# Kernel tuning notes

Hardware: AMD Instinct MI355X
Metric: run time of the kernel (lower is better)

Reference implementation:

```python
import jax, jax.numpy as jnp
import numpy as np

N_NODES = 100000
N_EDGES = 1600000
IN_C = 128
HID = 128
OUT_C = 10
N_GRAPHS = 512


def setup_inputs() -> dict:
    key = jax.random.key(0)
    ks = jax.random.split(key, 12)
    x = jax.random.normal(ks[0], (N_NODES, IN_C), dtype=jnp.float32)
    edge_index = jax.random.randint(ks[1], (2, N_EDGES), 0, N_NODES, dtype=jnp.int64)
    batch = jnp.sort(jax.random.randint(ks[2], (N_NODES,), 0, N_GRAPHS, dtype=jnp.int64))

    def lin(k, fan_in, fan_out):
        bound = 1.0 / np.sqrt(fan_in)
        return jax.random.uniform(k, (fan_in, fan_out), jnp.float32, -bound, bound)

    params = {
        # GraphConv layer i: W_rel (neighbor aggregate transform, with bias),
        # W_root (self transform, no bias) -- matches PyG GraphConv.
        "W1_rel": lin(ks[3], IN_C, HID), "b1": jnp.zeros((HID,), jnp.float32), "W1_root": lin(ks[4], IN_C, HID),
        "W2_rel": lin(ks[5], HID, HID), "b2": jnp.zeros((HID,), jnp.float32), "W2_root": lin(ks[6], HID, HID),
        "W3_rel": lin(ks[7], HID, HID), "b3": jnp.zeros((HID,), jnp.float32), "W3_root": lin(ks[8], HID, HID),
        "W_lin": lin(ks[9], HID, OUT_C), "b_lin": jnp.zeros((OUT_C,), jnp.float32),
    }
    return {"x": x, "edge_index": edge_index, "batch": batch, **params}


def _graph_conv(x, src, dst, W_rel, b, W_root):
    # PyG GraphConv with aggr='add': out_i = W_rel @ sum_{j->i} x_j + b + W_root @ x_i
    agg = jax.ops.segment_sum(x[src], dst, num_segments=x.shape[0])  # [N, d]
    return agg @ W_rel + b + x @ W_root


def reference(x, edge_index, batch,
              W1_rel, b1, W1_root,
              W2_rel, b2, W2_root,
              W3_rel, b3, W3_root,
              W_lin, b_lin):
    src, dst = edge_index[0], edge_index[1]
    h = jax.nn.relu(_graph_conv(x, src, dst, W1_rel, b1, W1_root))
    h = jax.nn.relu(_graph_conv(h, src, dst, W2_rel, b2, W2_root))
    h = _graph_conv(h, src, dst, W3_rel, b3, W3_root)
    # global mean pool over graphs
    sums = jax.ops.segment_sum(h, batch, num_segments=N_GRAPHS)             # [G, d]
    counts = jax.ops.segment_sum(jnp.ones((h.shape[0],), h.dtype), batch, num_segments=N_GRAPHS)
    pooled = sums / jnp.maximum(counts, 1.0)[:, None]
    return pooled @ W_lin + b_lin  # [G, OUT_C]
```

## Files before the change

### kernel.cpp

```cpp
#include <hip/hip_runtime.h>

static constexpr int NN = 100000;
static constexpr int NE = 1600000;
static constexpr int C  = 128;
static constexpr int OC = 10;
static constexpr int NG = 512;

static constexpr int BSH  = 9;
static constexpr int BNW  = 1 << BSH;
static constexpr int BK   = (NN + BNW - 1) / BNW;
static constexpr int BCAP = 12288;
static constexpr int EPB  = 8192;
static constexpr int ABLK = (NE + EPB - 1) / EPB;

static constexpr int TSTRIDE = 132;

typedef unsigned short u16;
typedef __attribute__((ext_vector_type(8))) short short8;
typedef __attribute__((ext_vector_type(8))) short bf16x8;
typedef __attribute__((ext_vector_type(4))) float f32x4;

__device__ __forceinline__ float bf2f(u16 u) {
    union { float f; unsigned int u32; } v; v.u32 = ((unsigned int)u) << 16; return v.f;
}
__device__ __forceinline__ u16 f2bf(float f) {
    union { float f; unsigned int u; } v; v.f = f;
    unsigned int u = v.u;
    unsigned int r = u + 0x7FFF + ((u >> 16) & 1);
    return (u16)(r >> 16);
}

__global__ __launch_bounds__(256) void k_binA(const int* __restrict__ src,
                                              const int* __restrict__ dst,
                                              int* __restrict__ gcnt,
                                              int* __restrict__ buck) {
    __shared__ int cnt[BK];
    __shared__ int curs[BK];
    int tid = threadIdx.x;
    for (int i = tid; i < BK; i += 256) cnt[i] = 0;
    __syncthreads();
    int e0 = blockIdx.x * EPB;
    for (int i = tid; i < EPB; i += 256) {
        int e = e0 + i;
        if (e < NE) atomicAdd(&cnt[dst[e] >> BSH], 1);
    }
    __syncthreads();
    for (int i = tid; i < BK; i += 256) {
        int c = cnt[i];
        int gb = (c > 0) ? atomicAdd(&gcnt[i], c) : 0;
        curs[i] = i * BCAP + gb;
    }
    __syncthreads();
    for (int i = tid; i < EPB; i += 256) {
        int e = e0 + i;
        if (e < NE) {
            int d = dst[e];
            int b = d >> BSH;
            int p = atomicAdd(&curs[b], 1);
            if (p < (b + 1) * BCAP)
                buck[p] = (src[e] << BSH) | (d & (BNW - 1));
        }
    }
}

__global__ void k_binscan(const int* __restrict__ gcnt, int* __restrict__ csrbase,
                          int* __restrict__ rp) {
    __shared__ int buf[256];
    int tid = threadIdx.x;
    int v = (tid < BK) ? gcnt[tid] : 0;
    buf[tid] = v;
    __syncthreads();
    for (int off = 1; off < 256; off <<= 1) {
        int t = (tid >= off) ? buf[tid - off] : 0;
        __syncthreads();
        buf[tid] += t;
        __syncthreads();
    }
    if (tid < BK) csrbase[tid] = buf[tid] - v;
    if (tid == 0) rp[NN] = NE;
}

__global__ __launch_bounds__(BNW) void k_binB(const int* __restrict__ gcnt,
                                              const int* __restrict__ csrbase,
                                              const int* __restrict__ buck,
                                              int* __restrict__ rp,
                                              int* __restrict__ csr) {
    int b = blockIdx.x;
    int tid = threadIdx.x;
    __shared__ int hist[BNW];
    __shared__ int scanbuf[BNW];
    int n = gcnt[b];
    if (n > BCAP) n = BCAP;
    int base = csrbase[b];
    const int* bb = buck + (size_t)b * BCAP;

    hist[tid] = 0;
    __syncthreads();
    for (int i = tid; i < n; i += BNW) atomicAdd(&hist[bb[i] & (BNW - 1)], 1);
    __syncthreads();

    int v = hist[tid];
    scanbuf[tid] = v;
    __syncthreads();
    for (int off = 1; off < BNW; off <<= 1) {
        int t = (tid >= off) ? scanbuf[tid - off] : 0;
        __syncthreads();
        scanbuf[tid] += t;
        __syncthreads();
    }
    int excl = scanbuf[tid] - v;
    int node = (b << BSH) + tid;
    if (node < NN) rp[node] = base + excl;
    __syncthreads();
    hist[tid] = base + excl;
    __syncthreads();
    for (int i = tid; i < n; i += BNW) {
        int en = bb[i];
        int p = atomicAdd(&hist[en & (BNW - 1)], 1);
        csr[p] = en >> BSH;
    }
}

__global__ void k_cvt_bf16(const float* __restrict__ in, u16* __restrict__ out) {
    int i = blockIdx.x * blockDim.x + threadIdx.x;
    size_t base = (size_t)i * 8;
    if (base >= (size_t)NN * C) return;
    float4 a = *reinterpret_cast<const float4*>(in + base);
    float4 b = *reinterpret_cast<const float4*>(in + base + 4);
    u16 o[8] = { f2bf(a.x), f2bf(a.y), f2bf(a.z), f2bf(a.w),
                 f2bf(b.x), f2bf(b.y), f2bf(b.z), f2bf(b.w) };
    *reinterpret_cast<short8*>(out + base) = *reinterpret_cast<const short8*>(o);
}

__global__ void k_pack_w(const float* __restrict__ W_rel,
                         const float* __restrict__ W_root,
                         u16* __restrict__ Bp) {
    int t = blockIdx.x * blockDim.x + threadIdx.x;
    if (t >= 4096) return;
    int lane = t & 63;
    int nfrag = (t >> 6) & 7;
    int kk = t >> 9;
    int col = nfrag * 16 + (lane & 15);
    int k0 = kk * 32 + (lane >> 4) * 8;
    u16 vals[8];
#pragma unroll
    for (int j = 0; j < 8; ++j) {
        int k = k0 + j;
        float w = (k < C) ? W_rel[k * C + col] : W_root[(k - C) * C + col];
        vals[j] = f2bf(w);
    }
    *reinterpret_cast<short8*>(Bp + (size_t)t * 8) = *reinterpret_cast<const short8*>(vals);
}

__global__ void k_gather(const u16* __restrict__ h, const int* __restrict__ rp,
                         const int* __restrict__ csr, u16* __restrict__ agg) {
    int t = blockIdx.x * blockDim.x + threadIdx.x;
    int node = t >> 4;
    if (node >= NN) return;
    int seg = (t & 15) * 8;
    int beg = rp[node], end = rp[node + 1];
    float acc[8] = {};
    int j = beg;
    for (; j + 4 <= end; j += 4) {
        int s0 = csr[j];
        int s1 = csr[j + 1];
        int s2 = csr[j + 2];
        int s3 = csr[j + 3];
        short8 v0 = *reinterpret_cast<const short8*>(h + (size_t)s0 * C + seg);
        short8 v1 = *reinterpret_cast<const short8*>(h + (size_t)s1 * C + seg);
        short8 v2 = *reinterpret_cast<const short8*>(h + (size_t)s2 * C + seg);
        short8 v3 = *reinterpret_cast<const short8*>(h + (size_t)s3 * C + seg);
#pragma unroll
        for (int q = 0; q < 8; ++q) {
            acc[q] += bf2f((u16)v0[q]);
            acc[q] += bf2f((u16)v1[q]);
            acc[q] += bf2f((u16)v2[q]);
            acc[q] += bf2f((u16)v3[q]);
        }
    }
    for (; j < end; ++j) {
        int s = csr[j];
        short8 v = *reinterpret_cast<const short8*>(h + (size_t)s * C + seg);
#pragma unroll
        for (int q = 0; q < 8; ++q) acc[q] += bf2f((u16)v[q]);
    }
    u16 o[8];
#pragma unroll
    for (int q = 0; q < 8; ++q) o[q] = f2bf(acc[q]);
    *reinterpret_cast<short8*>(agg + (size_t)node * C + seg) = *reinterpret_cast<const short8*>(o);
}

template <bool RELU>
__global__ __launch_bounds__(256) void k_transform_mfma(
    const u16* __restrict__ agg, const u16* __restrict__ h,
    const u16* __restrict__ Bp, const float* __restrict__ bias,
    u16* __restrict__ out) {
    __shared__ u16 tile[4][16 * TSTRIDE];
    int wave = threadIdx.x >> 6;
    int lane = threadIdx.x & 63;
    int row0 = blockIdx.x * 64 + wave * 16;
    int arow = row0 + (lane & 15);
    int rclamp = arow < NN ? arow : NN - 1;
    int koff = (lane >> 4) * 8;

    f32x4 acc[8] = {};
#pragma unroll
    for (int kk = 0; kk < 8; ++kk) {
        bf16x8 a;
        if (kk < 4) {
            a = *reinterpret_cast<const bf16x8*>(agg + (size_t)rclamp * C + kk * 32 + koff);
        } else {
            a = *reinterpret_cast<const bf16x8*>(h + (size_t)rclamp * C + (kk - 4) * 32 + koff);
        }
        const u16* bp = Bp + ((size_t)kk * 8 * 64 + lane) * 8;
#pragma unroll
        for (int n = 0; n < 8; ++n) {
            bf16x8 b = *reinterpret_cast<const bf16x8*>(bp + (size_t)n * 64 * 8);
            acc[n] = __builtin_amdgcn_mfma_f32_16x16x32_bf16(a, b, acc[n], 0, 0, 0);
        }
    }

    u16* T = tile[wave];
    int colbase = lane & 15;
    int rloc = (lane >> 4) * 4;
#pragma unroll
    for (int n = 0; n < 8; ++n) {
        int col = n * 16 + colbase;
        float bb = bias[col];
#pragma unroll
        for (int r = 0; r < 4; ++r) {
            float v = acc[n][r] + bb;
            if (RELU) v = fmaxf(v, 0.0f);
            T[(rloc + r) * TSTRIDE + col] = f2bf(v);
        }
    }
    __syncthreads();

#pragma unroll
    for (int k = 0; k < 4; ++k) {
        int idx = k * 64 + lane;
        int lr = idx >> 4;
        int off = (idx & 15) * 8;
        int ro = row0 + lr;
        if (ro < NN) {
            short8 v = *reinterpret_cast<const short8*>(&T[lr * TSTRIDE + off]);
            *reinterpret_cast<short8*>(out + (size_t)ro * C + off) = v;
        }
    }
}

__global__ void k_gbounds(const int* __restrict__ batch, int* __restrict__ gstart) {
    int g = blockIdx.x * blockDim.x + threadIdx.x;
    if (g > NG) return;
    int lo = 0, hi = NN;
    while (lo < hi) { int mid = (lo + hi) >> 1; if (batch[mid] < g) lo = mid + 1; else hi = mid; }
    gstart[g] = lo;
}

__global__ __launch_bounds__(256) void k_pool_final(
    const u16* __restrict__ h, const int* __restrict__ gstart,
    const float* __restrict__ W_lin, const float* __restrict__ b_lin,
    float* __restrict__ out) {
    int g = blockIdx.x;
    int rowslot = threadIdx.x >> 4;
    int seg = threadIdx.x & 15;
    int s = gstart[g], e = gstart[g + 1];

    float acc[8] = {};
    for (int i = s + rowslot; i < e; i += 16) {
        short8 v = *reinterpret_cast<const short8*>(h + (size_t)i * C + seg * 8);
#pragma unroll
        for (int q = 0; q < 8; ++q) acc[q] += bf2f((u16)v[q]);
    }

    __shared__ float red[16][C];
#pragma unroll
    for (int q = 0; q < 8; ++q) red[rowslot][seg * 8 + q] = acc[q];
    __syncthreads();

    __shared__ float sp[C];
    if (threadIdx.x < C) {
        float sum = 0.0f;
#pragma unroll
        for (int r = 0; r < 16; ++r) sum += red[r][threadIdx.x];
        float cnt = (float)max(e - s, 1);
        sp[threadIdx.x] = sum / cnt;
    }
    __syncthreads();
    if (threadIdx.x < OC) {
        float o = b_lin[threadIdx.x];
#pragma unroll 8
        for (int k = 0; k < C; ++k) o += sp[k] * W_lin[k * OC + threadIdx.x];
        out[g * OC + threadIdx.x] = o;
    }
}

extern "C" void kernel_launch(void* const* d_in, const int* in_sizes, int n_in,
                              void* d_out, int out_size, void* d_ws, size_t ws_size,
                              hipStream_t stream) {
    const float* x       = (const float*)d_in[0];
    const int*   eidx    = (const int*)d_in[1];
    const int*   batch   = (const int*)d_in[2];
    const float* W1_rel  = (const float*)d_in[3];
    const float* b1      = (const float*)d_in[4];
    const float* W1_root = (const float*)d_in[5];
    const float* W2_rel  = (const float*)d_in[6];
    const float* b2      = (const float*)d_in[7];
    const float* W2_root = (const float*)d_in[8];
    const float* W3_rel  = (const float*)d_in[9];
    const float* b3      = (const float*)d_in[10];
    const float* W3_root = (const float*)d_in[11];
    const float* W_lin   = (const float*)d_in[12];
    const float* b_lin   = (const float*)d_in[13];
    float* out = (float*)d_out;

    const int* src = eidx;
    const int* dst = eidx + NE;

    u16* xb   = (u16*)d_ws;
    u16* hb   = xb + (size_t)NN * C;
    u16* aggb = hb + (size_t)NN * C;
    u16* Bp   = aggb + (size_t)NN * C;
    int* rp      = (int*)(Bp + 3 * 32768);
    int* csr     = rp + NN + 1;
    int* buck    = csr + NE;
    int* gcnt    = buck + (size_t)BK * BCAP;
    int* csrbase = gcnt + BK;
    int* gstart  = csrbase + BK;

    const int gb = (NN * 16 + 255) / 256;
    const int tb = (NN + 63) / 64;
    const int cvtb = ((NN * C / 8) + 255) / 256;

    hipMemsetAsync(gcnt, 0, BK * sizeof(int), stream);
    k_binA<<<ABLK, 256, 0, stream>>>(src, dst, gcnt, buck);
    k_binscan<<<1, 256, 0, stream>>>(gcnt, csrbase, rp);
    k_binB<<<BK, BNW, 0, stream>>>(gcnt, csrbase, buck, rp, csr);

    k_cvt_bf16<<<cvtb, 256, 0, stream>>>(x, xb);
    k_pack_w<<<16, 256, 0, stream>>>(W1_rel, W1_root, Bp);
    k_pack_w<<<16, 256, 0, stream>>>(W2_rel, W2_root, Bp + 32768);
    k_pack_w<<<16, 256, 0, stream>>>(W3_rel, W3_root, Bp + 2 * 32768);
    k_gbounds<<<3, 256, 0, stream>>>(batch, gstart);

    k_gather<<<gb, 256, 0, stream>>>(xb, rp, csr, aggb);
    k_transform_mfma<true><<<tb, 256, 0, stream>>>(aggb, xb, Bp, b1, hb);

    k_gather<<<gb, 256, 0, stream>>>(hb, rp, csr, aggb);
    k_transform_mfma<true><<<tb, 256, 0, stream>>>(aggb, hb, Bp + 32768, b2, hb);

    k_gather<<<gb, 256, 0, stream>>>(hb, rp, csr, aggb);
    k_transform_mfma<false><<<tb, 256, 0, stream>>>(aggb, hb, Bp + 2 * 32768, b3, hb);

    k_pool_final<<<NG, 256, 0, stream>>>(hb, gstart, W_lin, b_lin, out);
}
```

Baseline: 343.2 us.

## Use a full wavefront per node in gather and merge small setup kernels

The gather kernel now assigns 64 lanes per node instead of 16. Four edge groups load neighbor rows in parallel, and the partial sums are combined with cross-lane shuffles before one quarter of the wave writes the result. This exposes more memory-level parallelism on the irregular neighbor gathers, in exchange for shuffle overhead and idle lanes on low-degree nodes. Separately, the bin scan is merged with the graph-bounds search, and the weight packing is merged with the bf16 conversion, which cuts the number of kernel launches.

```diff
diff --git a/kernel.cpp b/kernel.cpp
--- a/kernel.cpp
+++ b/kernel.cpp
@@ -63,21 +63,32 @@
     }
 }
 
-__global__ void k_binscan(const int* __restrict__ gcnt, int* __restrict__ csrbase,
-                          int* __restrict__ rp) {
-    __shared__ int buf[256];
+__global__ __launch_bounds__(256) void k_meta(const int* __restrict__ gcnt,
+                                              int* __restrict__ csrbase,
+                                              int* __restrict__ rp,
+                                              const int* __restrict__ batch,
+                                              int* __restrict__ gstart) {
     int tid = threadIdx.x;
-    int v = (tid < BK) ? gcnt[tid] : 0;
-    buf[tid] = v;
-    __syncthreads();
-    for (int off = 1; off < 256; off <<= 1) {
-        int t = (tid >= off) ? buf[tid - off] : 0;
+    if (blockIdx.x == 0) {
+        __shared__ int buf[256];
+        int v = (tid < BK) ? gcnt[tid] : 0;
+        buf[tid] = v;
         __syncthreads();
-        buf[tid] += t;
-        __syncthreads();
-    }
-    if (tid < BK) csrbase[tid] = buf[tid] - v;
-    if (tid == 0) rp[NN] = NE;
+        for (int off = 1; off < 256; off <<= 1) {
+            int t = (tid >= off) ? buf[tid - off] : 0;
+            __syncthreads();
+            buf[tid] += t;
+            __syncthreads();
+        }
+        if (tid < BK) csrbase[tid] = buf[tid] - v;
+        if (tid == 0) rp[NN] = NE;
+    } else {
+        int g = (blockIdx.x - 1) * 256 + tid;
+        if (g > NG) return;
+        int lo = 0, hi = NN;
+        while (lo < hi) { int mid = (lo + hi) >> 1; if (batch[mid] < g) lo = mid + 1; else hi = mid; }
+        gstart[g] = lo;
+    }
 }
 
 __global__ __launch_bounds__(BNW) void k_binB(const int* __restrict__ gcnt,
@@ -121,73 +132,98 @@
     }
 }
 
-__global__ void k_cvt_bf16(const float* __restrict__ in, u16* __restrict__ out) {
-    int i = blockIdx.x * blockDim.x + threadIdx.x;
-    size_t base = (size_t)i * 8;
-    if (base >= (size_t)NN * C) return;
-    float4 a = *reinterpret_cast<const float4*>(in + base);
-    float4 b = *reinterpret_cast<const float4*>(in + base + 4);
-    u16 o[8] = { f2bf(a.x), f2bf(a.y), f2bf(a.z), f2bf(a.w),
-                 f2bf(b.x), f2bf(b.y), f2bf(b.z), f2bf(b.w) };
-    *reinterpret_cast<short8*>(out + base) = *reinterpret_cast<const short8*>(o);
-}
-
-__global__ void k_pack_w(const float* __restrict__ W_rel,
-                         const float* __restrict__ W_root,
-                         u16* __restrict__ Bp) {
+__global__ __launch_bounds__(256) void k_prep(
+    const float* __restrict__ x, u16* __restrict__ xb,
+    const float* __restrict__ W1r, const float* __restrict__ W1o,
+    const float* __restrict__ W2r, const float* __restrict__ W2o,
+    const float* __restrict__ W3r, const float* __restrict__ W3o,
+    u16* __restrict__ Bp) {
+    int bid = blockIdx.x;
+    if (bid < 48) {
+        int layer = bid >> 4;
+        const float* Wr = (layer == 0) ? W1r : (layer == 1) ? W2r : W3r;
+        const float* Wo = (layer == 0) ? W1o : (layer == 1) ? W2o : W3o;
+        u16* out = Bp + layer * 32768;
+        int t = (bid & 15) * 256 + threadIdx.x;
+        int lane = t & 63;
+        int nfrag = (t >> 6) & 7;
+        int kk = t >> 9;
+        int col = nfrag * 16 + (lane & 15);
+        int k0 = kk * 32 + (lane >> 4) * 8;
+        u16 vals[8];
+#pragma unroll
+        for (int j = 0; j < 8; ++j) {
+            int k = k0 + j;
+            float w = (k < C) ? Wr[k * C + col] : Wo[(k - C) * C + col];
+            vals[j] = f2bf(w);
+        }
+        *reinterpret_cast<short8*>(out + (size_t)t * 8) = *reinterpret_cast<const short8*>(vals);
+    } else {
+        int i = (bid - 48) * 256 + threadIdx.x;
+        size_t base = (size_t)i * 8;
+        if (base >= (size_t)NN * C) return;
+        float4 a = *reinterpret_cast<const float4*>(x + base);
+        float4 b = *reinterpret_cast<const float4*>(x + base + 4);
+        u16 o[8] = { f2bf(a.x), f2bf(a.y), f2bf(a.z), f2bf(a.w),
+                     f2bf(b.x), f2bf(b.y), f2bf(b.z), f2bf(b.w) };
+        *reinterpret_cast<short8*>(xb + base) = *reinterpret_cast<const short8*>(o);
+    }
+}
+
+__global__ __launch_bounds__(256) void k_gather(const u16* __restrict__ h,
+                                                const int* __restrict__ rp,
+                                                const int* __restrict__ csr,
+                                                u16* __restrict__ agg) {
     int t = blockIdx.x * blockDim.x + threadIdx.x;
-    if (t >= 4096) return;
+    int node = t >> 6;
+    if (node >= NN) return;
     int lane = t & 63;
-    int nfrag = (t >> 6) & 7;
-    int kk = t >> 9;
-    int col = nfrag * 16 + (lane & 15);
-    int k0 = kk * 32 + (lane >> 4) * 8;
-    u16 vals[8];
-#pragma unroll
-    for (int j = 0; j < 8; ++j) {
-        int k = k0 + j;
-        float w = (k < C) ? W_rel[k * C + col] : W_root[(k - C) * C + col];
-        vals[j] = f2bf(w);
-    }
-    *reinterpret_cast<short8*>(Bp + (size_t)t * 8) = *reinterpret_cast<const short8*>(vals);
-}
-
-__global__ void k_gather(const u16* __restrict__ h, const int* __restrict__ rp,
-                         const int* __restrict__ csr, u16* __restrict__ agg) {
-    int t = blockIdx.x * blockDim.x + threadIdx.x;
-    int node = t >> 4;
-    if (node >= NN) return;
-    int seg = (t & 15) * 8;
+    int jj = lane >> 4;
+    int seg = (lane & 15) * 8;
     int beg = rp[node], end = rp[node + 1];
+
     float acc[8] = {};
-    int j = beg;
-    for (; j + 4 <= end; j += 4) {
-        int s0 = csr[j];
-        int s1 = csr[j + 1];
-        int s2 = csr[j + 2];
-        int s3 = csr[j + 3];
-        short8 v0 = *reinterpret_cast<const short8*>(h + (size_t)s0 * C + seg);
-        short8 v1 = *reinterpret_cast<const short8*>(h + (size_t)s1 * C + seg);
-        short8 v2 = *reinterpret_cast<const short8*>(h + (size_t)s2 * C + seg);
-        short8 v3 = *reinterpret_cast<const short8*>(h + (size_t)s3 * C + seg);
+    int j0 = beg;
+    for (; j0 + 8 <= end; j0 += 8) {
+        int sa = csr[j0 + jj];
+        int sb = csr[j0 + 4 + jj];
+        short8 va = *reinterpret_cast<const short8*>(h + (size_t)sa * C + seg);
+        short8 vb = *reinterpret_cast<const short8*>(h + (size_t)sb * C + seg);
 #pragma unroll
         for (int q = 0; q < 8; ++q) {
-            acc[q] += bf2f((u16)v0[q]);
-            acc[q] += bf2f((u16)v1[q]);
-            acc[q] += bf2f((u16)v2[q]);
-            acc[q] += bf2f((u16)v3[q]);
-        }
-    }
-    for (; j < end; ++j) {
-        int s = csr[j];
-        short8 v = *reinterpret_cast<const short8*>(h + (size_t)s * C + seg);
-#pragma unroll
-        for (int q = 0; q < 8; ++q) acc[q] += bf2f((u16)v[q]);
-    }
-    u16 o[8];
-#pragma unroll
-    for (int q = 0; q < 8; ++q) o[q] = f2bf(acc[q]);
-    *reinterpret_cast<short8*>(agg + (size_t)node * C + seg) = *reinterpret_cast<const short8*>(o);
+            acc[q] += bf2f((u16)va[q]);
+            acc[q] += bf2f((u16)vb[q]);
+        }
+    }
+    if (j0 < end) {
+        int ja = j0 + jj;
+        int jb = j0 + 4 + jj;
+        if (ja < end) {
+            int sa = csr[ja];
+            short8 va = *reinterpret_cast<const short8*>(h + (size_t)sa * C + seg);
+#pragma unroll
+            for (int q = 0; q < 8; ++q) acc[q] += bf2f((u16)va[q]);
+        }
+        if (jb < end) {
+            int sb = csr[jb];
+            short8 vb = *reinterpret_cast<const short8*>(h + (size_t)sb * C + seg);
+#pragma unroll
+            for (int q = 0; q < 8; ++q) acc[q] += bf2f((u16)vb[q]);
+        }
+    }
+
+#pragma unroll
+    for (int q = 0; q < 8; ++q) {
+        acc[q] += __shfl_xor(acc[q], 32);
+        acc[q] += __shfl_xor(acc[q], 16);
+    }
+    if (lane < 16) {
+        u16 o[8];
+#pragma unroll
+        for (int q = 0; q < 8; ++q) o[q] = f2bf(acc[q]);
+        *reinterpret_cast<short8*>(agg + (size_t)node * C + seg) =
+            *reinterpret_cast<const short8*>(o);
+    }
 }
 
 template <bool RELU>
@@ -247,14 +283,6 @@
             *reinterpret_cast<short8*>(out + (size_t)ro * C + off) = v;
         }
     }
-}
-
-__global__ void k_gbounds(const int* __restrict__ batch, int* __restrict__ gstart) {
-    int g = blockIdx.x * blockDim.x + threadIdx.x;
-    if (g > NG) return;
-    int lo = 0, hi = NN;
-    while (lo < hi) { int mid = (lo + hi) >> 1; if (batch[mid] < g) lo = mid + 1; else hi = mid; }
-    gstart[g] = lo;
 }
 
 __global__ __launch_bounds__(256) void k_pool_final(
@@ -328,20 +356,17 @@
     int* csrbase = gcnt + BK;
     int* gstart  = csrbase + BK;
 
-    const int gb = (NN * 16 + 255) / 256;
+    const int gb = (NN * 64 + 255) / 256;
     const int tb = (NN + 63) / 64;
-    const int cvtb = ((NN * C / 8) + 255) / 256;
+    const int prepb = 48 + ((NN * C / 8) + 255) / 256;
 
     hipMemsetAsync(gcnt, 0, BK * sizeof(int), stream);
     k_binA<<<ABLK, 256, 0, stream>>>(src, dst, gcnt, buck);
-    k_binscan<<<1, 256, 0, stream>>>(gcnt, csrbase, rp);
+    k_meta<<<4, 256, 0, stream>>>(gcnt, csrbase, rp, batch, gstart);
     k_binB<<<BK, BNW, 0, stream>>>(gcnt, csrbase, buck, rp, csr);
 
-    k_cvt_bf16<<<cvtb, 256, 0, stream>>>(x, xb);
-    k_pack_w<<<16, 256, 0, stream>>>(W1_rel, W1_root, Bp);
-    k_pack_w<<<16, 256, 0, stream>>>(W2_rel, W2_root, Bp + 32768);
-    k_pack_w<<<16, 256, 0, stream>>>(W3_rel, W3_root, Bp + 2 * 32768);
-    k_gbounds<<<3, 256, 0, stream>>>(batch, gstart);
+    k_prep<<<prepb, 256, 0, stream>>>(x, xb, W1_rel, W1_root, W2_rel, W2_root,
+                                      W3_rel, W3_root, Bp);
 
     k_gather<<<gb, 256, 0, stream>>>(xb, rp, csr, aggb);
     k_transform_mfma<true><<<tb, 256, 0, stream>>>(aggb, xb, Bp, b1, hb);
```

Result: faster. 335.0 us (-2.4%).
